# Kernel tuning notes

Hardware: AMD Instinct MI355X
Metric: run time of the kernel (lower is better)

Reference implementation:

```python
import jax, jax.numpy as jnp
import numpy as np

B, N, C, E, H = 2, 20000, 64, 640000, 16

def setup_inputs() -> dict:
    key = jax.random.key(0)
    ks = jax.random.split(key, 9)
    Q = jax.random.normal(ks[0], (B, N, C), dtype=jnp.float32)
    K = jax.random.normal(ks[1], (B, N, C), dtype=jnp.float32)
    V = jax.random.normal(ks[2], (B, N, C), dtype=jnp.float32)
    src = jax.random.randint(ks[3], (E,), 0, N, dtype=jnp.int32)
    dst = jax.random.randint(ks[4], (E,), 0, N, dtype=jnp.int32)
    efeat = jax.random.uniform(ks[5], (E, 2), dtype=jnp.float32)  # [s_norm, d_norm] in [0,1]
    W1 = jax.random.normal(ks[6], (2, H), dtype=jnp.float32) * 0.5
    b1 = jnp.zeros((H,), dtype=jnp.float32)
    W2 = jax.random.normal(ks[7], (H, 1), dtype=jnp.float32) * 0.5
    b2 = jnp.zeros((1,), dtype=jnp.float32)
    return {"Q": Q, "K": K, "V": V, "efeat": efeat, "W1": W1, "b1": b1,
            "W2": W2, "b2": b2, "src": src, "dst": dst}

def reference(Q, K, V, efeat, W1, b1, W2, b2, src, dst):
    n = Q.shape[1]
    # per-edge bias: MLP(e_ij) -> (E,)
    bias = (jax.nn.relu(efeat @ W1 + b1) @ W2 + b2)[:, 0]
    # per-edge logits: Q_dst . K_src  -> (E, B)
    logits = jnp.einsum('bec,bec->eb', Q[:, dst, :], K[:, src, :]) + bias[:, None]
    # segment softmax over incoming edges of each dst node
    seg_max = jax.ops.segment_max(logits, dst, num_segments=n)          # (N, B)
    exp_l = jnp.exp(logits - seg_max[dst])                               # (E, B)
    denom = jax.ops.segment_sum(exp_l, dst, num_segments=n)[dst]         # (E, B)
    alpha = exp_l / denom                                                # (E, B)
    # weighted aggregation of parent values: (E,B,C) scattered to (N,B,C)
    msg = alpha[:, :, None] * jnp.transpose(V[:, src, :], (1, 0, 2))
    H_msg = jax.ops.segment_sum(msg, dst, num_segments=n)                # (N, B, C)
    return jnp.transpose(H_msg, (1, 0, 2))                               # (B, N, C)
```

## Files before the change

kernel.cpp:

```cpp
#include <hip/hip_runtime.h>
#include <hip/hip_fp16.h>
#include <math.h>


#define EB_B 2
#define EB_C 64
#define EB_H 16
#define EB_CAP 80

typedef _Float16 h2v __attribute__((ext_vector_type(2)));

__device__ __forceinline__ unsigned f2h2(float a, float b) {
    __half2 h = __floats2half2_rn(a, b);
    return *reinterpret_cast<unsigned*>(&h);
}
__device__ __forceinline__ float2 h2f2(unsigned u) {
    __half2 h = *reinterpret_cast<__half2*>(&u);
    return __half22float2(h);
}
__device__ __forceinline__ h2v bch2(unsigned u) {
    h2v r;
    __builtin_memcpy(&r, &u, 4);
    return r;
}

template <int CTRL>
__device__ __forceinline__ float dpp_add(float x) {
    int y = __builtin_amdgcn_update_dpp(0, __float_as_int(x), CTRL, 0xf, 0xf, true);
    return x + __int_as_float(y);
}
__device__ __forceinline__ float row16_allsum(float x) {
    x = dpp_add<0xB1>(x);
    x = dpp_add<0x4E>(x);
    x = dpp_add<0x124>(x);
    x = dpp_add<0x128>(x);
    return x;
}

__global__ __launch_bounds__(256) void eb_pack(
    const float4* __restrict__ K4, const float4* __restrict__ V4,
    uint4* __restrict__ kv, int total,
    int* __restrict__ cnt, int N) {
    int i = blockIdx.x * blockDim.x + threadIdx.x;
    if (i < N) cnt[i] = 0;
    if (i >= total) return;
    float4 k = K4[i];
    float4 v = V4[i];
    uint4 o;
    o.x = f2h2(k.x, k.y); o.y = f2h2(k.z, k.w);
    o.z = f2h2(v.x, v.y); o.w = f2h2(v.z, v.w);
    kv[i] = o;
}

__global__ __launch_bounds__(256) void eb_fillcount(
    const int* __restrict__ dst, const int* __restrict__ src,
    const float2* __restrict__ efeat2,
    const float* __restrict__ W1, const float* __restrict__ b1,
    const float* __restrict__ W2, const float* __restrict__ b2,
    int* __restrict__ cnt, unsigned* __restrict__ ep, int E) {
    int e = blockIdx.x * blockDim.x + threadIdx.x;
    if (e >= E) return;
    float2 ef = efeat2[e];
    float acc = b2[0];
#pragma unroll
    for (int h = 0; h < EB_H; ++h) {
        float a = fmaf(ef.x, W1[h], fmaf(ef.y, W1[EB_H + h], b1[h]));
        a = fmaxf(a, 0.0f);
        acc = fmaf(a, W2[h], acc);
    }
    int d = dst[e];
    int slot = atomicAdd(&cnt[d], 1);
    if (slot < EB_CAP) {
        unsigned hb = f2h2(0.0f, acc) & 0xffff0000u;
        ep[d * EB_CAP + slot] = (unsigned)src[e] | hb;
    }
}

__global__ __launch_bounds__(256) void eb_attn_fp16(
    const float4* __restrict__ Q4, const uint4* __restrict__ kv,
    const unsigned* __restrict__ ep, const int* __restrict__ cnt,
    float4* __restrict__ out4, int N) {
    int wave = threadIdx.x >> 6;
    int lane = threadIdx.x & 63;
    int task = blockIdx.x * 4 + wave;
    if (task >= N * EB_B) return;
    int b = (task >= N) ? 1 : 0;
    int n = task - (b ? N : 0);
    int g = lane >> 4;
    int cl = lane & 15;
    const size_t brow = (size_t)N * 16;
    float4 qf = Q4[(size_t)b * brow + (size_t)n * 16 + cl];
    h2v q01; q01[0] = (_Float16)qf.x; q01[1] = (_Float16)qf.y;
    h2v q23; q23[0] = (_Float16)qf.z; q23[1] = (_Float16)qf.w;
    const uint4* kvb = kv + (size_t)b * brow;
    int deg = cnt[n];
    deg = (deg > EB_CAP) ? EB_CAP : deg;
    int start = n * EB_CAP;
    int end = start + deg;
    int nit = (deg + 7) >> 3;

    int eP = start + g;
    unsigned c0 = ep[eP < end ? eP : start];
    unsigned c1 = ep[eP + 4 < end ? eP + 4 : start];
    uint4 u0 = kvb[(size_t)(c0 & 0xffffu) * 16 + cl];
    uint4 u1 = kvb[(size_t)(c1 & 0xffffu) * 16 + cl];
    int eN = start + 8 + g;
    unsigned n0 = ep[eN < end ? eN : start];
    unsigned n1 = ep[eN + 4 < end ? eN + 4 : start];

    float s = 0.0f;
    float ax = 0.0f, ay = 0.0f, az = 0.0f, aw = 0.0f;

    for (int it = 0; it < nit; ++it) {
        uint4 fu0 = kvb[(size_t)(n0 & 0xffffu) * 16 + cl];
        uint4 fu1 = kvb[(size_t)(n1 & 0xffffu) * 16 + cl];
        int e2 = start + (it + 2) * 8 + g;
        unsigned nn0 = ep[e2 < end ? e2 : start];
        unsigned nn1 = ep[e2 + 4 < end ? e2 + 4 : start];
        int e0 = start + it * 8 + g;
        int e1 = e0 + 4;
        bool v0 = e0 < end;
        bool v1 = e1 < end;
        float p0 = __builtin_amdgcn_fdot2(q01, bch2(u0.x),
                   __builtin_amdgcn_fdot2(q23, bch2(u0.y), 0.0f, false), false);
        float p1 = __builtin_amdgcn_fdot2(q01, bch2(u1.x),
                   __builtin_amdgcn_fdot2(q23, bch2(u1.y), 0.0f, false), false);
        p0 = row16_allsum(p0);
        p1 = row16_allsum(p1);
        float b0 = h2f2(c0).y;
        float b1_ = h2f2(c1).y;
        float l0 = fminf(p0 + b0, 80.0f);
        float l1 = fminf(p1 + b1_, 80.0f);
        float w0 = v0 ? __expf(l0) : 0.0f;
        float w1 = v1 ? __expf(l1) : 0.0f;
        float2 va0 = h2f2(u0.z), vb0 = h2f2(u0.w);
        float2 va1 = h2f2(u1.z), vb1 = h2f2(u1.w);
        s += w0 + w1;
        ax = fmaf(w0, va0.x, fmaf(w1, va1.x, ax));
        ay = fmaf(w0, va0.y, fmaf(w1, va1.y, ay));
        az = fmaf(w0, vb0.x, fmaf(w1, vb1.x, az));
        aw = fmaf(w0, vb0.y, fmaf(w1, vb1.y, aw));
        c0 = n0; c1 = n1; u0 = fu0; u1 = fu1; n0 = nn0; n1 = nn1;
    }

    s  += __shfl_xor(s, 16);  s  += __shfl_xor(s, 32);
    ax += __shfl_xor(ax, 16); ax += __shfl_xor(ax, 32);
    ay += __shfl_xor(ay, 16); ay += __shfl_xor(ay, 32);
    az += __shfl_xor(az, 16); az += __shfl_xor(az, 32);
    aw += __shfl_xor(aw, 16); aw += __shfl_xor(aw, 32);

    if (lane < 16) {
        float inv = (deg > 0) ? 1.0f / s : 0.0f;
        float4 o;
        o.x = ax * inv; o.y = ay * inv; o.z = az * inv; o.w = aw * inv;
        out4[(size_t)b * brow + (size_t)n * 16 + cl] = o;
    }
}

__global__ __launch_bounds__(256) void eb_attn_f32(
    const float4* __restrict__ Q4, const float4* __restrict__ K4,
    const float4* __restrict__ V4,
    const unsigned* __restrict__ ep, const int* __restrict__ cnt,
    float4* __restrict__ out4, int N) {
    int wave = threadIdx.x >> 6;
    int lane = threadIdx.x & 63;
    int task = blockIdx.x * 4 + wave;
    if (task >= N * EB_B) return;
    int b = (task >= N) ? 1 : 0;
    int n = task - (b ? N : 0);
    int g = lane >> 4;
    int cl = lane & 15;
    const size_t brow = (size_t)N * 16;
    float4 q = Q4[(size_t)b * brow + (size_t)n * 16 + cl];
    const float4* Kb = K4 + (size_t)b * brow;
    const float4* Vb = V4 + (size_t)b * brow;
    int deg = cnt[n];
    deg = (deg > EB_CAP) ? EB_CAP : deg;
    int start = n * EB_CAP;
    int end = start + deg;
    int nit = (deg + 3) >> 2;
    float s = 0.0f;
    float ax = 0.0f, ay = 0.0f, az = 0.0f, aw = 0.0f;
    for (int it = 0; it < nit; ++it) {
        int ei = start + it * 4 + g;
        bool valid = ei < end;
        unsigned md = ep[valid ? ei : start];
        int sv = md & 0xffffu;
        float4 k = Kb[(size_t)sv * 16 + cl];
        float4 v = Vb[(size_t)sv * 16 + cl];
        float p = fmaf(q.x, k.x, fmaf(q.y, k.y, fmaf(q.z, k.z, q.w * k.w)));
        p = row16_allsum(p);
        float l = fminf(p + h2f2(md).y, 80.0f);
        float w = valid ? __expf(l) : 0.0f;
        s += w;
        ax = fmaf(w, v.x, ax);
        ay = fmaf(w, v.y, ay);
        az = fmaf(w, v.z, az);
        aw = fmaf(w, v.w, aw);
    }
    s  += __shfl_xor(s, 16);  s  += __shfl_xor(s, 32);
    ax += __shfl_xor(ax, 16); ax += __shfl_xor(ax, 32);
    ay += __shfl_xor(ay, 16); ay += __shfl_xor(ay, 32);
    az += __shfl_xor(az, 16); az += __shfl_xor(az, 32);
    aw += __shfl_xor(aw, 16); aw += __shfl_xor(aw, 32);
    if (lane < 16) {
        float inv = (deg > 0) ? 1.0f / s : 0.0f;
        float4 o;
        o.x = ax * inv; o.y = ay * inv; o.z = az * inv; o.w = aw * inv;
        out4[(size_t)b * brow + (size_t)n * 16 + cl] = o;
    }
}

extern "C" void kernel_launch(void* const* d_in, const int* in_sizes, int n_in,
                              void* d_out, int out_size, void* d_ws, size_t ws_size,
                              hipStream_t stream) {
    const float4* Q4  = (const float4*)d_in[0];
    const float4* K4  = (const float4*)d_in[1];
    const float4* V4  = (const float4*)d_in[2];
    const float2* ef2 = (const float2*)d_in[3];
    const float* W1   = (const float*)d_in[4];
    const float* b1   = (const float*)d_in[5];
    const float* W2   = (const float*)d_in[6];
    const float* b2   = (const float*)d_in[7];
    const int*   src  = (const int*)d_in[8];
    const int*   dst  = (const int*)d_in[9];
    float4* out4 = (float4*)d_out;

    const int E = in_sizes[8];
    const int N = in_sizes[0] / (EB_B * EB_C);
    const int total = EB_B * N * 16;

    char* base = (char*)d_ws;
    size_t off = 0;
    auto take = [&](size_t nbytes) {
        char* p = base + off;
        off += (nbytes + 15) & ~(size_t)15;
        return p;
    };
    int* cnt     = (int*)take((size_t)N * 4);
    unsigned* ep = (unsigned*)take((size_t)N * EB_CAP * 4);
    uint4* kv    = (uint4*)take((size_t)total * 16);
    bool use_fp16 = off <= ws_size;

    const int tpb = 256;
    eb_pack<<<(total + tpb - 1) / tpb, tpb, 0, stream>>>(
        K4, V4, kv, use_fp16 ? total : 0, cnt, N);
    eb_fillcount<<<(E + tpb - 1) / tpb, tpb, 0, stream>>>(
        dst, src, ef2, W1, b1, W2, b2, cnt, ep, E);

    int tasks = N * EB_B;
    int blks = (tasks + 3) / 4;
    if (use_fp16) {
        eb_attn_fp16<<<blks, tpb, 0, stream>>>(Q4, kv, ep, cnt, out4, N);
    } else {
        eb_attn_f32<<<blks, tpb, 0, stream>>>(Q4, K4, V4, ep, cnt, out4, N);
    }
}
```

Before: 81.33 us.

## Move edge slot atomics into the pack kernel and store slots separately

The per-destination atomic counting moves out of the fill kernel and into the K/V pack kernel, which now records each edge's slot in a new workspace array. The counter array is zeroed with a separate memset. The fill kernel then only computes the edge MLP bias and scatters entries using the precomputed slots. The aim is to overlap the atomic traffic with the fp16 pack streaming. The cost is an extra memset launch plus writing and reading an E-sized slot array.

Result: slower. 85.98 us (+5.7%).

```diff
diff --git a/kernel.cpp b/kernel.cpp
--- a/kernel.cpp
+++ b/kernel.cpp
@@ -37,27 +37,30 @@
     return x;
 }
 
-__global__ __launch_bounds__(256) void eb_pack(
+__global__ __launch_bounds__(256) void eb_count_pack(
+    const int* __restrict__ dst, int* __restrict__ cnt,
+    int* __restrict__ slot,
     const float4* __restrict__ K4, const float4* __restrict__ V4,
-    uint4* __restrict__ kv, int total,
-    int* __restrict__ cnt, int N) {
+    uint4* __restrict__ kv, int total, int E) {
     int i = blockIdx.x * blockDim.x + threadIdx.x;
-    if (i < N) cnt[i] = 0;
-    if (i >= total) return;
-    float4 k = K4[i];
-    float4 v = V4[i];
-    uint4 o;
-    o.x = f2h2(k.x, k.y); o.y = f2h2(k.z, k.w);
-    o.z = f2h2(v.x, v.y); o.w = f2h2(v.z, v.w);
-    kv[i] = o;
-}
-
-__global__ __launch_bounds__(256) void eb_fillcount(
+    if (i < E) slot[i] = atomicAdd(&cnt[dst[i]], 1);
+    if (i < total) {
+        float4 k = K4[i];
+        float4 v = V4[i];
+        uint4 o;
+        o.x = f2h2(k.x, k.y); o.y = f2h2(k.z, k.w);
+        o.z = f2h2(v.x, v.y); o.w = f2h2(v.z, v.w);
+        kv[i] = o;
+    }
+}
+
+__global__ __launch_bounds__(256) void eb_fill(
     const int* __restrict__ dst, const int* __restrict__ src,
+    const int* __restrict__ slot,
     const float2* __restrict__ efeat2,
     const float* __restrict__ W1, const float* __restrict__ b1,
     const float* __restrict__ W2, const float* __restrict__ b2,
-    int* __restrict__ cnt, unsigned* __restrict__ ep, int E) {
+    unsigned* __restrict__ ep, int E) {
     int e = blockIdx.x * blockDim.x + threadIdx.x;
     if (e >= E) return;
     float2 ef = efeat2[e];
@@ -69,10 +72,10 @@
         acc = fmaf(a, W2[h], acc);
     }
     int d = dst[e];
-    int slot = atomicAdd(&cnt[d], 1);
-    if (slot < EB_CAP) {
+    int s = slot[e];
+    if (s < EB_CAP) {
         unsigned hb = f2h2(0.0f, acc) & 0xffff0000u;
-        ep[d * EB_CAP + slot] = (unsigned)src[e] | hb;
+        ep[d * EB_CAP + s] = (unsigned)src[e] | hb;
     }
 }
 
@@ -238,15 +241,18 @@
         return p;
     };
     int* cnt     = (int*)take((size_t)N * 4);
+    int* slot    = (int*)take((size_t)E * 4);
     unsigned* ep = (unsigned*)take((size_t)N * EB_CAP * 4);
     uint4* kv    = (uint4*)take((size_t)total * 16);
     bool use_fp16 = off <= ws_size;
 
     const int tpb = 256;
-    eb_pack<<<(total + tpb - 1) / tpb, tpb, 0, stream>>>(
-        K4, V4, kv, use_fp16 ? total : 0, cnt, N);
-    eb_fillcount<<<(E + tpb - 1) / tpb, tpb, 0, stream>>>(
-        dst, src, ef2, W1, b1, W2, b2, cnt, ep, E);
+    hipMemsetAsync(cnt, 0, (size_t)N * sizeof(int), stream);
+    int span = (E > total) ? E : total;
+    eb_count_pack<<<(span + tpb - 1) / tpb, tpb, 0, stream>>>(
+        dst, cnt, slot, K4, V4, kv, use_fp16 ? total : 0, E);
+    eb_fill<<<(E + tpb - 1) / tpb, tpb, 0, stream>>>(
+        dst, src, slot, ef2, W1, b1, W2, b2, ep, E);
 
     int tasks = N * EB_B;
     int blks = (tasks + 3) / 4;
```
